# Kernel tuning notes

Hardware: AMD Instinct MI355X
Metric: run time of the kernel (lower is better)

## Reference

```python
import jax, jax.numpy as jnp
import numpy as np

B, D, T, H, K = 16, 1024, 1024, 1024, 2  # batch, in_channels, seq_len, hidden_size, kernel_size


def setup_inputs() -> dict:
    key = jax.random.key(0)
    k1, k2, k3 = jax.random.split(key, 3)
    inputs = jax.random.normal(k1, (B, D, T), dtype=jnp.float32)
    # Conv1D kernel in OIH layout: [3H, D, K]; scaled to keep gates in a sane range
    conv_w = jax.random.normal(k2, (3 * H, D, K), dtype=jnp.float32) / np.float32(np.sqrt(D * K))
    conv_b = jax.random.normal(k3, (3 * H,), dtype=jnp.float32) * 0.01
    return {"inputs": inputs, "conv_w": conv_w, "conv_b": conv_b}


def reference(inputs, conv_w, conv_b):
    # inputs: [B, D, T] (channels_first, as in the keras call signature)
    # Causal conv: left-pad time by K-1, then VALID conv -> [B, 3H, T]
    padded = jnp.pad(inputs, ((0, 0), (0, 0), (K - 1, 0)))
    gates = jax.lax.conv_general_dilated(
        padded, conv_w, window_strides=(1,), padding="VALID",
        dimension_numbers=("NCH", "OIH", "NCH"))
    gates = gates + conv_b[None, :, None]
    gates = jnp.transpose(gates, (0, 2, 1))  # [B, T, 3H]
    z = jnp.tanh(gates[..., :H])
    f = jax.nn.sigmoid(gates[..., H:2 * H])
    o = jax.nn.sigmoid(gates[..., 2 * H:])

    # fo-pooling linear recurrence: c_t = f_t * c_{t-1} + (1 - f_t) * z_t, c_0 = 0
    zf = (jnp.transpose(z, (1, 0, 2)), jnp.transpose(f, (1, 0, 2)))  # time-major [T, B, H]

    def step(c, zf_t):
        z_t, f_t = zf_t
        c_new = f_t * c + (1.0 - f_t) * z_t
        return c_new, c_new

    c0 = jnp.zeros((B, H), dtype=inputs.dtype)
    _, c_seq = jax.lax.scan(step, c0, zf)
    c_seq = jnp.transpose(c_seq, (1, 0, 2))  # [B, T, H]
    h_seq = o * c_seq
    return c_seq, h_seq
```

## Files before the change

kernel.cpp:

```cpp
#include <hip/hip_runtime.h>

#define Bsz 16
#define Dch 1024
#define Tsz 1024
#define Hsz 1024
#define Mtot (Bsz*Tsz)
#define K2   (2*Dch)
#define Ntot (3*Hsz)

typedef __attribute__((ext_vector_type(8))) short bf16x8;
typedef __attribute__((ext_vector_type(4))) float f32x4;
typedef __attribute__((ext_vector_type(8))) unsigned short u16x8;

__device__ __forceinline__ unsigned short f2bf(float x) {
    unsigned u = __float_as_uint(x);
    u += 0x7FFFu + ((u >> 16) & 1u);
    return (unsigned short)(u >> 16);
}
__device__ __forceinline__ float bf2f(unsigned short s) {
    return __uint_as_float(((unsigned)s) << 16);
}

__global__ void prep_w(const float* __restrict__ w, unsigned short* __restrict__ wb) {
    int i = blockIdx.x * blockDim.x + threadIdx.x;
    float4 v = ((const float4*)w)[i];
    ushort4 r;
    r.x = f2bf(v.x); r.y = f2bf(v.y); r.z = f2bf(v.z); r.w = f2bf(v.w);
    ((ushort4*)wb)[i] = r;
}

__global__ void prep_a(const float* __restrict__ x, unsigned short* __restrict__ a2) {
    __shared__ float Xs[64][66];
    int bid = blockIdx.x;
    int b   = bid >> 8;
    int tt0 = ((bid >> 4) & 15) << 6;
    int dd0 = (bid & 15) << 6;
    int tid  = threadIdx.x;
    int colt = tid & 63, rowq = tid >> 6;
    const size_t xbase = (size_t)b * (Dch * Tsz);
    #pragma unroll
    for (int r = 0; r < 16; r++) {
        int dd = r * 4 + rowq;
        Xs[dd][1 + colt] = x[xbase + (size_t)(dd0 + dd) * Tsz + tt0 + colt];
    }
    if (tid < 64) {
        Xs[tid][0] = (tt0 == 0) ? 0.f : x[xbase + (size_t)(dd0 + tid) * Tsz + tt0 - 1];
    }
    __syncthreads();
    #pragma unroll
    for (int r = 0; r < 16; r++) {
        int tr = r * 4 + rowq;
        int dc = colt;
        float v0 = Xs[dc][tr];
        float v1 = Xs[dc][tr + 1];
        unsigned pack = (unsigned)f2bf(v0) | ((unsigned)f2bf(v1) << 16);
        int m = (b << 10) + tt0 + tr;
        ((unsigned*)a2)[(size_t)m * (K2 / 2) + dd0 + dc] = pack;
    }
}

#define LDK 72
__global__ __launch_bounds__(256)
void gemm_gates(const unsigned short* __restrict__ A, const unsigned short* __restrict__ Bt,
                const float* __restrict__ bias,
                float* __restrict__ zc, float* __restrict__ fh, unsigned short* __restrict__ ob) {
    __shared__ __align__(16) unsigned short As[128 * LDK];
    __shared__ __align__(16) unsigned short Bs2[128 * LDK];
    int tid = threadIdx.x;
    int n0 = blockIdx.x << 7;
    int m0 = blockIdx.y << 7;
    int wave = tid >> 6, lane = tid & 63;
    int wm = wave & 1, wn = wave >> 1;
    int lm = lane & 15, q = lane >> 4;
    f32x4 acc[4][4] = {};
    const size_t abase = (size_t)m0 * K2;
    const size_t bbase = (size_t)n0 * K2;
    for (int kb = 0; kb < K2; kb += 64) {
        #pragma unroll
        for (int i = 0; i < 4; i++) {
            int lid = i * 256 + tid;
            int row = lid >> 3;
            int col = (lid & 7) << 3;
            *(u16x8*)&As[row * LDK + col]  = *(const u16x8*)&A[abase + (size_t)row * K2 + kb + col];
            *(u16x8*)&Bs2[row * LDK + col] = *(const u16x8*)&Bt[bbase + (size_t)row * K2 + kb + col];
        }
        __syncthreads();
        #pragma unroll
        for (int ks = 0; ks < 64; ks += 32) {
            bf16x8 af[4], bfr[4];
            #pragma unroll
            for (int i = 0; i < 4; i++)
                af[i] = *(bf16x8*)&As[(wm * 64 + i * 16 + lm) * LDK + ks + q * 8];
            #pragma unroll
            for (int j = 0; j < 4; j++)
                bfr[j] = *(bf16x8*)&Bs2[(wn * 64 + j * 16 + lm) * LDK + ks + q * 8];
            #pragma unroll
            for (int i = 0; i < 4; i++)
                #pragma unroll
                for (int j = 0; j < 4; j++)
                    acc[i][j] = __builtin_amdgcn_mfma_f32_16x16x32_bf16(af[i], bfr[j], acc[i][j], 0, 0, 0);
        }
        __syncthreads();
    }
    int gt = n0 >> 10;
    #pragma unroll
    for (int i = 0; i < 4; i++) {
        int mrow = m0 + wm * 64 + i * 16 + q * 4;
        #pragma unroll
        for (int j = 0; j < 4; j++) {
            int n = n0 + wn * 64 + j * 16 + lm;
            float bv = bias[n];
            int hcol = n & 1023;
            #pragma unroll
            for (int r = 0; r < 4; r++) {
                float g = acc[i][j][r] + bv;
                size_t idx = (size_t)(mrow + r) * Hsz + hcol;
                if (gt == 0) {
                    float e = __expf(2.f * g);
                    zc[idx] = __fdividef(e - 1.f, e + 1.f);
                } else {
                    float s = __fdividef(1.f, 1.f + __expf(-g));
                    if (gt == 1) fh[idx] = s;
                    else         ob[idx] = f2bf(s);
                }
            }
        }
    }
}

__global__ __launch_bounds__(64)
void recurrence(float* __restrict__ zc, float* __restrict__ fh,
                const unsigned short* __restrict__ ob) {
    int g = blockIdx.x * 64 + threadIdx.x;
    int b = g >> 10, h = g & 1023;
    size_t base = ((size_t)b << 20) + h;
    float c = 0.f;
    #pragma unroll 8
    for (int t = 0; t < Tsz; t++) {
        size_t idx = base + ((size_t)t << 10);
        float z = zc[idx];
        float f = fh[idx];
        float o = bf2f(ob[idx]);
        c = z + f * (c - z);
        zc[idx] = c;
        fh[idx] = o * c;
    }
}

extern "C" void kernel_launch(void* const* d_in, const int* in_sizes, int n_in,
                              void* d_out, int out_size, void* d_ws, size_t ws_size,
                              hipStream_t stream) {
    const float* x    = (const float*)d_in[0];
    const float* w    = (const float*)d_in[1];
    const float* bias = (const float*)d_in[2];
    float* zc = (float*)d_out;
    float* fh = (float*)d_out + (size_t)Mtot * Hsz;
    unsigned short* a2 = (unsigned short*)d_ws;
    unsigned short* wb = a2 + (size_t)Mtot * K2;
    unsigned short* ob = wb + (size_t)Ntot * K2;

    hipLaunchKernelGGL(prep_w, dim3(6144), dim3(256), 0, stream, w, wb);
    hipLaunchKernelGGL(prep_a, dim3(4096), dim3(256), 0, stream, x, a2);
    hipLaunchKernelGGL(gemm_gates, dim3(24, 128), dim3(256), 0, stream, a2, wb, bias, zc, fh, ob);
    hipLaunchKernelGGL(recurrence, dim3(256), dim3(64), 0, stream, zc, fh, ob);
}
```

Baseline: 557.7 us.

## Chunk the time recurrence into three-pass scan and use direct global-to-LDS loads

Measured after the change: 517.6 us. 7.2% less time.

```diff
diff --git a/kernel.cpp b/kernel.cpp
--- a/kernel.cpp
+++ b/kernel.cpp
@@ -7,10 +7,11 @@
 #define Mtot (Bsz*Tsz)
 #define K2   (2*Dch)
 #define Ntot (3*Hsz)
+#define NCH  16
+#define CL   64
 
 typedef __attribute__((ext_vector_type(8))) short bf16x8;
 typedef __attribute__((ext_vector_type(4))) float f32x4;
-typedef __attribute__((ext_vector_type(8))) unsigned short u16x8;
 
 __device__ __forceinline__ unsigned short f2bf(float x) {
     unsigned u = __float_as_uint(x);
@@ -20,6 +21,10 @@
 __device__ __forceinline__ float bf2f(unsigned short s) {
     return __uint_as_float(((unsigned)s) << 16);
 }
+
+#define GLOAD_LDS16(gp, lp) \
+    __builtin_amdgcn_global_load_lds((const __attribute__((address_space(1))) void*)(gp), \
+                                     (__attribute__((address_space(3))) void*)(lp), 16, 0, 0)
 
 __global__ void prep_w(const float* __restrict__ w, unsigned short* __restrict__ wb) {
     int i = blockIdx.x * blockDim.x + threadIdx.x;
@@ -59,41 +64,44 @@
     }
 }
 
-#define LDK 72
 __global__ __launch_bounds__(256)
 void gemm_gates(const unsigned short* __restrict__ A, const unsigned short* __restrict__ Bt,
                 const float* __restrict__ bias,
                 float* __restrict__ zc, float* __restrict__ fh, unsigned short* __restrict__ ob) {
-    __shared__ __align__(16) unsigned short As[128 * LDK];
-    __shared__ __align__(16) unsigned short Bs2[128 * LDK];
+    __shared__ __align__(16) unsigned short As[128 * 64];
+    __shared__ __align__(16) unsigned short Bs2[128 * 64];
     int tid = threadIdx.x;
     int n0 = blockIdx.x << 7;
     int m0 = blockIdx.y << 7;
     int wave = tid >> 6, lane = tid & 63;
     int wm = wave & 1, wn = wave >> 1;
     int lm = lane & 15, q = lane >> 4;
+
+    int lrow = lane >> 3, lchunk = lane & 7;
+    int gch  = lchunk ^ lrow;
+    const unsigned short* Ag = A  + (size_t)(m0 + wave * 32 + lrow) * K2 + gch * 8;
+    const unsigned short* Bg = Bt + (size_t)(n0 + wave * 32 + lrow) * K2 + gch * 8;
+
     f32x4 acc[4][4] = {};
-    const size_t abase = (size_t)m0 * K2;
-    const size_t bbase = (size_t)n0 * K2;
     for (int kb = 0; kb < K2; kb += 64) {
         #pragma unroll
-        for (int i = 0; i < 4; i++) {
-            int lid = i * 256 + tid;
-            int row = lid >> 3;
-            int col = (lid & 7) << 3;
-            *(u16x8*)&As[row * LDK + col]  = *(const u16x8*)&A[abase + (size_t)row * K2 + kb + col];
-            *(u16x8*)&Bs2[row * LDK + col] = *(const u16x8*)&Bt[bbase + (size_t)row * K2 + kb + col];
+        for (int j = 0; j < 4; j++) {
+            int rbase = wave * 32 + j * 8;
+            GLOAD_LDS16(Ag + (size_t)j * 8 * K2 + kb, &As[rbase * 64]);
+            GLOAD_LDS16(Bg + (size_t)j * 8 * K2 + kb, &Bs2[rbase * 64]);
         }
         __syncthreads();
         #pragma unroll
         for (int ks = 0; ks < 64; ks += 32) {
             bf16x8 af[4], bfr[4];
+            int cs = ks >> 3;
+            int sw = (lm & 7);
             #pragma unroll
             for (int i = 0; i < 4; i++)
-                af[i] = *(bf16x8*)&As[(wm * 64 + i * 16 + lm) * LDK + ks + q * 8];
+                af[i] = *(bf16x8*)&As[(wm * 64 + i * 16 + lm) * 64 + (((cs + q) ^ sw) << 3)];
             #pragma unroll
             for (int j = 0; j < 4; j++)
-                bfr[j] = *(bf16x8*)&Bs2[(wn * 64 + j * 16 + lm) * LDK + ks + q * 8];
+                bfr[j] = *(bf16x8*)&Bs2[(wn * 64 + j * 16 + lm) * 64 + (((cs + q) ^ sw) << 3)];
             #pragma unroll
             for (int i = 0; i < 4; i++)
                 #pragma unroll
@@ -128,16 +136,50 @@
     }
 }
 
-__global__ __launch_bounds__(64)
-void recurrence(float* __restrict__ zc, float* __restrict__ fh,
-                const unsigned short* __restrict__ ob) {
-    int g = blockIdx.x * 64 + threadIdx.x;
+__global__ __launch_bounds__(256)
+void scan1(const float* __restrict__ zc, const float* __restrict__ fh,
+           float* __restrict__ Aw, float* __restrict__ Bw) {
+    int blk = blockIdx.x;
+    int hb = blk & 3, ch = (blk >> 2) & 15, b = blk >> 6;
+    int h = hb * 256 + threadIdx.x;
+    size_t base = ((size_t)b << 20) + ((size_t)(ch * CL) << 10) + h;
+    float a = 1.f, bb = 0.f;
+    #pragma unroll 8
+    for (int s = 0; s < CL; s++) {
+        size_t idx = base + ((size_t)s << 10);
+        float z = zc[idx], f = fh[idx];
+        a *= f;
+        bb = z + f * (bb - z);
+    }
+    int o = (ch * Bsz + b) * Hsz + h;
+    Aw[o] = a; Bw[o] = bb;
+}
+
+__global__ __launch_bounds__(256)
+void scan2(const float* __restrict__ Aw, const float* __restrict__ Bw,
+           float* __restrict__ C0) {
+    int g = blockIdx.x * 256 + threadIdx.x;
     int b = g >> 10, h = g & 1023;
-    size_t base = ((size_t)b << 20) + h;
     float c = 0.f;
+    #pragma unroll
+    for (int ch = 0; ch < NCH; ch++) {
+        int o = (ch * Bsz + b) * Hsz + h;
+        C0[o] = c;
+        c = Aw[o] * c + Bw[o];
+    }
+}
+
+__global__ __launch_bounds__(256)
+void scan3(float* __restrict__ zc, float* __restrict__ fh,
+           const unsigned short* __restrict__ ob, const float* __restrict__ C0) {
+    int blk = blockIdx.x;
+    int hb = blk & 3, ch = (blk >> 2) & 15, b = blk >> 6;
+    int h = hb * 256 + threadIdx.x;
+    size_t base = ((size_t)b << 20) + ((size_t)(ch * CL) << 10) + h;
+    float c = C0[(ch * Bsz + b) * Hsz + h];
     #pragma unroll 8
-    for (int t = 0; t < Tsz; t++) {
-        size_t idx = base + ((size_t)t << 10);
+    for (int s = 0; s < CL; s++) {
+        size_t idx = base + ((size_t)s << 10);
         float z = zc[idx];
         float f = fh[idx];
         float o = bf2f(ob[idx]);
@@ -158,9 +200,14 @@
     unsigned short* a2 = (unsigned short*)d_ws;
     unsigned short* wb = a2 + (size_t)Mtot * K2;
     unsigned short* ob = wb + (size_t)Ntot * K2;
+    float* Aw = (float*)(ob + (size_t)Mtot * Hsz);
+    float* Bw = Aw + NCH * Bsz * Hsz;
+    float* C0 = Bw + NCH * Bsz * Hsz;
 
     hipLaunchKernelGGL(prep_w, dim3(6144), dim3(256), 0, stream, w, wb);
     hipLaunchKernelGGL(prep_a, dim3(4096), dim3(256), 0, stream, x, a2);
     hipLaunchKernelGGL(gemm_gates, dim3(24, 128), dim3(256), 0, stream, a2, wb, bias, zc, fh, ob);
-    hipLaunchKernelGGL(recurrence, dim3(256), dim3(64), 0, stream, zc, fh, ob);
-}
+    hipLaunchKernelGGL(scan1, dim3(1024), dim3(256), 0, stream, zc, fh, Aw, Bw);
+    hipLaunchKernelGGL(scan2, dim3(64), dim3(256), 0, stream, Aw, Bw, C0);
+    hipLaunchKernelGGL(scan3, dim3(1024), dim3(256), 0, stream, zc, fh, ob, C0);
+}
```
